# Kernel tuning notes

Hardware: AMD Instinct MI355X
Metric: run time of the kernel (lower is better)

The kernel has to match this reference:

```python
import jax, jax.numpy as jnp
import numpy as np

NUM_CAT = 16          # num_cat_features
NUM_ATTR = 144        # num_attribute_features
NUM_NUMERICS = NUM_ATTR - NUM_CAT  # 128
N_ARY = 32            # n_ary_num_features (k = min(32, 128) = 32)
NUM_SEGMENTS = 100000 # static stand-in for cat_max+1 (idx values in [0,100000))
N_ROWS = 1000000


def setup_inputs() -> dict:
    key = jax.random.key(0)
    k1, k2, k3, k4 = jax.random.split(key, 4)
    return {
        "inputs": jax.random.normal(k1, (N_ROWS, NUM_ATTR), dtype=jnp.float32),
        "idx_inputs": jax.random.randint(k2, (N_ROWS, NUM_CAT), 0, NUM_SEGMENTS, dtype=jnp.int64),
        "cat_mask": jax.random.uniform(k3, (NUM_CAT,), dtype=jnp.float32),
        "numeric_mask": jax.random.uniform(k4, (NUM_NUMERICS,), dtype=jnp.float32),
    }


def reference(inputs, idx_inputs, cat_mask, numeric_mask):
    # 1) pick the GroupBy categorical column via softmax + top-1
    cm = jax.nn.softmax(cat_mask)
    top_cat_val, top_cat_idx = jax.lax.top_k(cm, 1)            # ([1], [1])
    cat_idx = jnp.take(idx_inputs, top_cat_idx[0], axis=1)     # [N] int

    # 2) scatter-add numeric features grouped by the chosen category
    updates = inputs[:, NUM_CAT:]                              # [N, NUM_NUMERICS]
    agg = jax.ops.segment_sum(updates, cat_idx, num_segments=NUM_SEGMENTS)  # [S, NUM_NUMERICS]

    # 3) gather the per-group aggregate back to each row
    gathered = agg[cat_idx]                                    # [N, NUM_NUMERICS]

    # 4) top-k numeric-feature selection, scaled by mask confidence
    nm = jax.nn.softmax(numeric_mask)
    top_num_val, top_num_idx = jax.lax.top_k(nm, N_ARY)        # ([K], [K])
    conf = (top_num_val + top_cat_val) / 2.0                   # [K] (top_cat_val broadcasts)
    return gathered[:, top_num_idx] * conf[None, :]            # [N, K]
```

## Files before the change

kernel.cpp:

```cpp
#include <hip/hip_runtime.h>

#define NUM_CAT 16
#define NUM_ATTR 144
#define NUM_NUM 128
#define N_ARY 32
#define NUM_SEG 100000
#define N_ROWS 1000000

#define AGG_OFFSET 512

__global__ void setup_kernel(const float* __restrict__ cat_mask,
                             const float* __restrict__ num_mask,
                             int* __restrict__ hdr_i,
                             float* __restrict__ hdr_f) {
    __shared__ float s_cm[NUM_CAT];
    __shared__ float s_x[NUM_NUM];
    __shared__ float s_p[NUM_NUM];
    const int tid = threadIdx.x;

    if (tid < NUM_CAT) s_cm[tid] = cat_mask[tid];
    float x = num_mask[tid];
    s_x[tid] = x;
    __syncthreads();

    float nmax = s_x[0];
    #pragma unroll 8
    for (int i = 1; i < NUM_NUM; ++i) nmax = fmaxf(nmax, s_x[i]);
    float e = expf(x - nmax);
    s_p[tid] = e;
    __syncthreads();
    float nsum = 0.f;
    #pragma unroll 8
    for (int i = 0; i < NUM_NUM; ++i) nsum += s_p[i];
    float inv = 1.0f / nsum;
    float p = e * inv;
    __syncthreads();
    s_p[tid] = p;
    __syncthreads();

    float cmax = s_cm[0]; int cidx = 0;
    #pragma unroll
    for (int i = 1; i < NUM_CAT; ++i) {
        float v = s_cm[i];
        if (v > cmax) { cmax = v; cidx = i; }
    }
    float csum = 0.f;
    #pragma unroll
    for (int i = 0; i < NUM_CAT; ++i) csum += expf(s_cm[i] - cmax);
    float top_cat_val = 1.0f / csum;

    int rank = 0;
    #pragma unroll 8
    for (int j = 0; j < NUM_NUM; ++j) {
        float pj = s_p[j];
        rank += (pj > p) || (pj == p && j < tid);
    }
    if (rank < N_ARY) {
        hdr_i[rank] = NUM_CAT + tid;
        hdr_f[32 + rank] = 0.5f * (p + top_cat_val);
    }
    if (tid == 0) hdr_i[64] = cidx;
}

__global__ void accum_kernel(const float* __restrict__ inputs,
                             const int* __restrict__ idx,
                             const int* __restrict__ hdr_i,
                             float* __restrict__ agg) {
    const int j = threadIdx.x & 31;
    const int col = hdr_i[j];
    const int topcat = hdr_i[64];
    const int total = N_ROWS * 32;
    int t = blockIdx.x * blockDim.x + threadIdx.x;
    const int stride = gridDim.x * blockDim.x;
    for (; t < total; t += stride) {
        int row = t >> 5;
        int seg = idx[row * NUM_CAT + topcat];
        float v = inputs[row * NUM_ATTR + col];
        atomicAdd(&agg[seg * 32 + j], v);
    }
}

__global__ void gather_kernel(const int* __restrict__ idx,
                              const int* __restrict__ hdr_i,
                              const float* __restrict__ hdr_f,
                              const float* __restrict__ agg,
                              float* __restrict__ out) {
    const int j = threadIdx.x & 31;
    const float cf = hdr_f[32 + j];
    const int topcat = hdr_i[64];
    const int total = N_ROWS * 32;
    int t = blockIdx.x * blockDim.x + threadIdx.x;
    const int stride = gridDim.x * blockDim.x;
    for (; t < total; t += stride) {
        int row = t >> 5;
        int seg = idx[row * NUM_CAT + topcat];
        out[t] = agg[seg * 32 + j] * cf;
    }
}

extern "C" void kernel_launch(void* const* d_in, const int* in_sizes, int n_in,
                              void* d_out, int out_size, void* d_ws, size_t ws_size,
                              hipStream_t stream) {
    const float* inputs   = (const float*)d_in[0];
    const int*   idx      = (const int*)d_in[1];
    const float* cat_mask = (const float*)d_in[2];
    const float* num_mask = (const float*)d_in[3];
    float* out = (float*)d_out;

    int*   hdr_i = (int*)d_ws;
    float* hdr_f = (float*)d_ws;
    float* agg   = (float*)((char*)d_ws + AGG_OFFSET);

    setup_kernel<<<1, 128, 0, stream>>>(cat_mask, num_mask, hdr_i, hdr_f);

    hipMemsetAsync(agg, 0, (size_t)NUM_SEG * 32 * sizeof(float), stream);

    accum_kernel<<<8192, 256, 0, stream>>>(inputs, idx, hdr_i, agg);

    gather_kernel<<<8192, 256, 0, stream>>>(idx, hdr_i, hdr_f, agg, out);
}
```

Before: 858.9 us.

## Accumulate into column-major aggregate, transpose, and cache per-row segment ids

Atomic adds now target a feature-major aggregate buffer, which a new tiled transpose kernel converts back to segment-major before the gather. The accumulation pass also writes the chosen segment index per row to a compact array, so the gather no longer reads the strided idx matrix. The layout change spreads the 32 atomics for a row across separate cache lines, which may reduce same-line contention but loses coalescing. It adds an extra kernel and an extra 12.8MB buffer pass.

```diff
diff --git a/kernel.cpp b/kernel.cpp
--- a/kernel.cpp
+++ b/kernel.cpp
@@ -7,7 +7,9 @@
 #define NUM_SEG 100000
 #define N_ROWS 1000000
 
-#define AGG_OFFSET 512
+#define AGG2_OFFSET 512
+#define AGG_OFFSET  (AGG2_OFFSET + (size_t)NUM_SEG * 32 * 4)
+#define SEGC_OFFSET (AGG2_OFFSET + 2 * (size_t)NUM_SEG * 32 * 4)
 
 __global__ void setup_kernel(const float* __restrict__ cat_mask,
                              const float* __restrict__ num_mask,
@@ -65,7 +67,8 @@
 __global__ void accum_kernel(const float* __restrict__ inputs,
                              const int* __restrict__ idx,
                              const int* __restrict__ hdr_i,
-                             float* __restrict__ agg) {
+                             float* __restrict__ agg2,
+                             int* __restrict__ segc) {
     const int j = threadIdx.x & 31;
     const int col = hdr_i[j];
     const int topcat = hdr_i[64];
@@ -76,24 +79,44 @@
         int row = t >> 5;
         int seg = idx[row * NUM_CAT + topcat];
         float v = inputs[row * NUM_ATTR + col];
-        atomicAdd(&agg[seg * 32 + j], v);
+        atomicAdd(&agg2[j * NUM_SEG + seg], v);
+        if (j == 0) segc[row] = seg;
     }
 }
 
-__global__ void gather_kernel(const int* __restrict__ idx,
-                              const int* __restrict__ hdr_i,
+__global__ void transpose_kernel(const float* __restrict__ agg2,
+                                 float* __restrict__ agg) {
+    __shared__ float tile[32][64 + 1];
+    const int s0 = blockIdx.x * 64;
+    const int ts = threadIdx.x & 63;
+    const int tj = threadIdx.x >> 6;
+    #pragma unroll
+    for (int j = tj; j < 32; j += 4) {
+        int s = s0 + ts;
+        tile[j][ts] = (s < NUM_SEG) ? agg2[j * NUM_SEG + s] : 0.f;
+    }
+    __syncthreads();
+    const int wj = threadIdx.x & 31;
+    const int ws = threadIdx.x >> 5;
+    #pragma unroll
+    for (int s = ws; s < 64; s += 8) {
+        int seg = s0 + s;
+        if (seg < NUM_SEG) agg[seg * 32 + wj] = tile[wj][s];
+    }
+}
+
+__global__ void gather_kernel(const int* __restrict__ segc,
                               const float* __restrict__ hdr_f,
                               const float* __restrict__ agg,
                               float* __restrict__ out) {
     const int j = threadIdx.x & 31;
     const float cf = hdr_f[32 + j];
-    const int topcat = hdr_i[64];
     const int total = N_ROWS * 32;
     int t = blockIdx.x * blockDim.x + threadIdx.x;
     const int stride = gridDim.x * blockDim.x;
     for (; t < total; t += stride) {
         int row = t >> 5;
-        int seg = idx[row * NUM_CAT + topcat];
+        int seg = segc[row];
         out[t] = agg[seg * 32 + j] * cf;
     }
 }
@@ -109,13 +132,17 @@
 
     int*   hdr_i = (int*)d_ws;
     float* hdr_f = (float*)d_ws;
+    float* agg2  = (float*)((char*)d_ws + AGG2_OFFSET);
     float* agg   = (float*)((char*)d_ws + AGG_OFFSET);
+    int*   segc  = (int*)((char*)d_ws + SEGC_OFFSET);
 
     setup_kernel<<<1, 128, 0, stream>>>(cat_mask, num_mask, hdr_i, hdr_f);
 
-    hipMemsetAsync(agg, 0, (size_t)NUM_SEG * 32 * sizeof(float), stream);
+    hipMemsetAsync(agg2, 0, (size_t)NUM_SEG * 32 * sizeof(float), stream);
 
-    accum_kernel<<<8192, 256, 0, stream>>>(inputs, idx, hdr_i, agg);
+    accum_kernel<<<8192, 256, 0, stream>>>(inputs, idx, hdr_i, agg2, segc);
 
-    gather_kernel<<<8192, 256, 0, stream>>>(idx, hdr_i, hdr_f, agg, out);
+    transpose_kernel<<<(NUM_SEG + 63) / 64, 256, 0, stream>>>(agg2, agg);
+
+    gather_kernel<<<8192, 256, 0, stream>>>(segc, hdr_f, agg, out);
 }
```

Result: slower. 2.217 ms (+158.1%).

## Replace float atomic scatter-add with counting-sort by segment and per-segment reduce

Applied to the files above, without the earlier changes.

Replaces the per-element float atomicAdd aggregation and separate gather with a counting sort of rows by segment: histogram, single-block prefix scan, atomic placement, then one warp per segment that sums its rows and writes the scaled result back to each row. This removes 32M contended float atomics and the agg table round trip. In exchange it adds several small kernels, a serial single-block scan, and scattered row reads and writes in the reduce phase. Summation order within a segment now depends on placement order, which is nondeterministic.

```diff
diff --git a/kernel.cpp b/kernel.cpp
--- a/kernel.cpp
+++ b/kernel.cpp
@@ -7,7 +7,10 @@
 #define NUM_SEG 100000
 #define N_ROWS 1000000
 
-#define AGG_OFFSET 512
+#define CNT_OFFSET   (1u << 20)
+#define OFS_OFFSET   (2u << 20)
+#define SEGC_OFFSET  (4u << 20)
+#define ORDER_OFFSET (8u << 20)
 
 __global__ void setup_kernel(const float* __restrict__ cat_mask,
                              const float* __restrict__ num_mask,
@@ -62,39 +65,82 @@
     if (tid == 0) hdr_i[64] = cidx;
 }
 
-__global__ void accum_kernel(const float* __restrict__ inputs,
-                             const int* __restrict__ idx,
-                             const int* __restrict__ hdr_i,
-                             float* __restrict__ agg) {
-    const int j = threadIdx.x & 31;
-    const int col = hdr_i[j];
+__global__ void hist_kernel(const int* __restrict__ idx,
+                            const int* __restrict__ hdr_i,
+                            int* __restrict__ segc,
+                            int* __restrict__ cnt) {
     const int topcat = hdr_i[64];
-    const int total = N_ROWS * 32;
-    int t = blockIdx.x * blockDim.x + threadIdx.x;
+    int r = blockIdx.x * blockDim.x + threadIdx.x;
     const int stride = gridDim.x * blockDim.x;
-    for (; t < total; t += stride) {
-        int row = t >> 5;
-        int seg = idx[row * NUM_CAT + topcat];
-        float v = inputs[row * NUM_ATTR + col];
-        atomicAdd(&agg[seg * 32 + j], v);
+    for (; r < N_ROWS; r += stride) {
+        int seg = idx[r * NUM_CAT + topcat];
+        segc[r] = seg;
+        atomicAdd(&cnt[seg], 1);
     }
 }
 
-__global__ void gather_kernel(const int* __restrict__ idx,
-                              const int* __restrict__ hdr_i,
-                              const float* __restrict__ hdr_f,
-                              const float* __restrict__ agg,
-                              float* __restrict__ out) {
+#define SCAN_T 1024
+#define SCAN_CHUNK 98
+__global__ void scan_kernel(const int* __restrict__ cnt,
+                            int* __restrict__ ofs) {
+    __shared__ int s[SCAN_T];
+    const int t = threadIdx.x;
+    const int lo = t * SCAN_CHUNK;
+    int hi = lo + SCAN_CHUNK; if (hi > NUM_SEG) hi = NUM_SEG;
+    int sum = 0;
+    for (int i = lo; i < hi; ++i) sum += cnt[i];
+    s[t] = sum;
+    __syncthreads();
+    for (int d = 1; d < SCAN_T; d <<= 1) {
+        int v = 0;
+        if (t >= d) v = s[t - d];
+        __syncthreads();
+        if (t >= d) s[t] += v;
+        __syncthreads();
+    }
+    int run = (t > 0) ? s[t - 1] : 0;
+    for (int i = lo; i < hi; ++i) {
+        ofs[i] = run;
+        run += cnt[i];
+    }
+}
+
+__global__ void place_kernel(const int* __restrict__ segc,
+                             int* __restrict__ ofs,
+                             int* __restrict__ order) {
+    int r = blockIdx.x * blockDim.x + threadIdx.x;
+    const int stride = gridDim.x * blockDim.x;
+    for (; r < N_ROWS; r += stride) {
+        int seg = segc[r];
+        int pos = atomicAdd(&ofs[seg], 1);
+        order[pos] = r;
+    }
+}
+
+#define SEGS_PER_BLOCK 8
+__global__ void reduce_scatter_kernel(const float* __restrict__ inputs,
+                                      const int* __restrict__ order,
+                                      const int* __restrict__ cnt,
+                                      const int* __restrict__ ofs_end,
+                                      const int* __restrict__ hdr_i,
+                                      const float* __restrict__ hdr_f,
+                                      float* __restrict__ out) {
+    const int seg = blockIdx.x * SEGS_PER_BLOCK + (threadIdx.x >> 5);
     const int j = threadIdx.x & 31;
+    const int col = hdr_i[j];
     const float cf = hdr_f[32 + j];
-    const int topcat = hdr_i[64];
-    const int total = N_ROWS * 32;
-    int t = blockIdx.x * blockDim.x + threadIdx.x;
-    const int stride = gridDim.x * blockDim.x;
-    for (; t < total; t += stride) {
-        int row = t >> 5;
-        int seg = idx[row * NUM_CAT + topcat];
-        out[t] = agg[seg * 32 + j] * cf;
+    const int end = ofs_end[seg];
+    const int n = cnt[seg];
+    const int start = end - n;
+    float acc = 0.f;
+    for (int r = 0; r < n; ++r) {
+        int row = order[start + r];
+        acc += inputs[row * NUM_ATTR + col];
+    }
+    const float ov = acc * cf;
+    for (int r = 0; r < n; ++r) {
+        int row = order[start + r];
+        out[row * 32 + j] = ov;
     }
 }
 
@@ -109,13 +155,21 @@
 
     int*   hdr_i = (int*)d_ws;
     float* hdr_f = (float*)d_ws;
-    float* agg   = (float*)((char*)d_ws + AGG_OFFSET);
+    int*   cnt   = (int*)((char*)d_ws + CNT_OFFSET);
+    int*   ofs   = (int*)((char*)d_ws + OFS_OFFSET);
+    int*   segc  = (int*)((char*)d_ws + SEGC_OFFSET);
+    int*   order = (int*)((char*)d_ws + ORDER_OFFSET);
 
     setup_kernel<<<1, 128, 0, stream>>>(cat_mask, num_mask, hdr_i, hdr_f);
 
-    hipMemsetAsync(agg, 0, (size_t)NUM_SEG * 32 * sizeof(float), stream);
+    hipMemsetAsync(cnt, 0, (size_t)NUM_SEG * sizeof(int), stream);
 
-    accum_kernel<<<8192, 256, 0, stream>>>(inputs, idx, hdr_i, agg);
+    hist_kernel<<<2048, 256, 0, stream>>>(idx, hdr_i, segc, cnt);
 
-    gather_kernel<<<8192, 256, 0, stream>>>(idx, hdr_i, hdr_f, agg, out);
+    scan_kernel<<<1, SCAN_T, 0, stream>>>(cnt, ofs);
+
+    place_kernel<<<2048, 256, 0, stream>>>(segc, ofs, order);
+
+    reduce_scatter_kernel<<<NUM_SEG / SEGS_PER_BLOCK, 256, 0, stream>>>(
+        inputs, order, cnt, ofs, hdr_i, hdr_f, out);
 }
```

Result: slower. 1.089 ms (+26.8%).
